# Optimization experiments

Hardware: AMD Instinct MI355X
Metric: run time of the kernel (lower is better)

The kernel has to match this reference:

```python
import jax, jax.numpy as jnp
import numpy as np

N_HEADS = 8
D_K = 64
NEG = 1e9


def setup_inputs() -> dict:
    key = jax.random.key(0)
    k1, k2, k3 = jax.random.split(key, 3)
    B, L, C = 4, 2048, 512
    x = jax.random.normal(k1, (B, L, C), dtype=jnp.float32)
    W_in = jax.random.normal(k2, (C, N_HEADS * D_K * 3), dtype=jnp.float32) * (C ** -0.5)
    b_in = jnp.zeros((N_HEADS * D_K * 3,), dtype=jnp.float32)
    W_out = jax.random.normal(k3, (N_HEADS * D_K, C), dtype=jnp.float32) * ((N_HEADS * D_K) ** -0.5)
    b_out = jnp.zeros((C,), dtype=jnp.float32)
    return {"x": x, "W_in": W_in, "b_in": b_in, "W_out": W_out, "b_out": b_out}


def reference(x, W_in, b_in, W_out, b_out):
    B, L, C = x.shape
    H, Dk = N_HEADS, D_K
    scale = Dk ** -0.5
    qkv = x @ W_in + b_in                       # [B, L, 3*H*Dk]
    qkv = qkv.reshape(B, L, H, 3 * Dk)
    q, k, v = jnp.split(qkv, 3, axis=-1)         # each [B, L, H, Dk]
    attn = jnp.einsum('bihd,bjhd->bijh', q, k) * scale  # [B, L, L, H]
    mask = jnp.tril(jnp.ones((L, L), dtype=x.dtype))[None, :, :, None]
    attn = attn * mask - NEG * (1.0 - mask)
    attn = jax.nn.softmax(attn, axis=2)          # softmax over j
    res = jnp.einsum('bijh,bjhd->bihd', attn, v)  # [B, L, H, Dk]
    res = res.reshape(B, L, H * Dk)
    res = res @ W_out + b_out
    return res + x
```

## Files before the change

kernel.cpp:

```cpp
#include <hip/hip_runtime.h>
#include <hip/hip_bf16.h>
#include <math.h>
#include <cstddef>
#include <cstring>


constexpr int B_SZ  = 4;
constexpr int L_SEQ = 2048;
constexpr int C_DIM = 512;
constexpr int H_N   = 8;
constexpr int DK    = 64;
constexpr int N_QKV = 1536;
constexpr int M_ROWS = B_SZ * L_SEQ;
constexpr float QSCALE = 0.125f * 1.44269504088896f;
constexpr float DEFER_THR = 11.5f;

typedef __attribute__((ext_vector_type(4))) float f32x4;
typedef __attribute__((ext_vector_type(8))) short bf16x8;

static __device__ inline ushort f2bf(float f) {
  unsigned u = __builtin_bit_cast(unsigned, f);
  u += 0x7fffu + ((u >> 16) & 1u);
  return (ushort)(u >> 16);
}

static __device__ inline unsigned pack_bf2(float a, float b) {
  const __hip_bfloat162 v = __float22bfloat162_rn(make_float2(a, b));
  unsigned u;
  __builtin_memcpy(&u, &v, 4);
  return u;
}

typedef __attribute__((address_space(1))) const unsigned int* gas1_t;
typedef __attribute__((address_space(3))) unsigned int* las3_t;
static __device__ inline void gload_lds16(const void* g, void* l) {
  __builtin_amdgcn_global_load_lds((gas1_t)g, (las3_t)l, 16, 0, 0);
}


__global__ __launch_bounds__(256) void convert_bf16(
    const float* __restrict__ src, ushort* __restrict__ dst, int n4) {
  const int i = blockIdx.x * 256 + threadIdx.x;
  if (i < n4) {
    const float4 v = reinterpret_cast<const float4*>(src)[i];
    ushort4 o;
    o.x = f2bf(v.x); o.y = f2bf(v.y); o.z = f2bf(v.z); o.w = f2bf(v.w);
    reinterpret_cast<ushort4*>(dst)[i] = o;
  }
}

__global__ __launch_bounds__(256) void transpose_bf16(
    const float* __restrict__ src, ushort* __restrict__ dst, int R, int C) {
  __shared__ ushort T[64][65];
  const int c0 = blockIdx.x * 64, r0 = blockIdx.y * 64;
#pragma unroll
  for (int p = 0; p < 16; ++p) {
    const int idx = threadIdx.x + p * 256;
    const int r = idx >> 6, c = idx & 63;
    T[r][c] = f2bf(src[(size_t)(r0 + r) * C + c0 + c]);
  }
  __syncthreads();
#pragma unroll
  for (int p = 0; p < 16; ++p) {
    const int idx = threadIdx.x + p * 256;
    const int r = idx >> 6, c = idx & 63;
    dst[(size_t)(c0 + r) * R + r0 + c] = T[c][r];
  }
}

template <int EPI>
__global__ __launch_bounds__(256) void gemm_bf16(
    const ushort* __restrict__ A, const ushort* __restrict__ Bt,
    const float* __restrict__ bias, ushort* __restrict__ Qo,
    ushort* __restrict__ Ko, ushort* __restrict__ Vto,
    float* __restrict__ outF, const float* __restrict__ resid,
    int N, int K) {
  __shared__ ushort Al[128 * 32];
  __shared__ ushort Bl[128 * 32];
  const int tid = threadIdx.x;
  const int w = tid >> 6, l = tid & 63;
  const int cc = l & 15, gg = l >> 4;
  const int bm = blockIdx.y * 128, bn = blockIdx.x * 128;
  const int wr = w >> 1, wc = w & 1;
  f32x4 acc[4][4] = {};

  for (int k0 = 0; k0 < K; k0 += 32) {
#pragma unroll
    for (int q = 0; q < 2; ++q) {
      const int cbase = q * 256 + w * 64;
      const int c = cbase + l;
      gload_lds16(A + (size_t)(bm + (c >> 2)) * K + k0 + (c & 3) * 8,
                  &Al[cbase * 8]);
      gload_lds16(Bt + (size_t)(bn + (c >> 2)) * K + k0 + (c & 3) * 8,
                  &Bl[cbase * 8]);
    }
    __syncthreads();
    bf16x8 aF[4], bF[4];
#pragma unroll
    for (int i = 0; i < 4; ++i)
      aF[i] = *reinterpret_cast<const bf16x8*>(
          &Al[(wr * 64 + i * 16 + cc) * 32 + gg * 8]);
#pragma unroll
    for (int j = 0; j < 4; ++j)
      bF[j] = *reinterpret_cast<const bf16x8*>(
          &Bl[(wc * 64 + j * 16 + cc) * 32 + gg * 8]);
#pragma unroll
    for (int i = 0; i < 4; ++i)
#pragma unroll
      for (int j = 0; j < 4; ++j)
        acc[i][j] = __builtin_amdgcn_mfma_f32_16x16x32_bf16(aF[i], bF[j],
                                                            acc[i][j], 0, 0, 0);
    __syncthreads();
  }

  if (EPI == 0) {
#pragma unroll
    for (int j = 0; j < 4; ++j) {
      const int colbase = bn + wc * 64 + j * 16;
      const int h = colbase / 192, rem = colbase % 192;
      const int type = rem / 64, d = (rem % 64) + cc;
      const float bv = bias[colbase + cc];
#pragma unroll
      for (int i = 0; i < 4; ++i) {
        const int rowbase = bm + wr * 64 + i * 16 + 4 * gg;
        const int b = rowbase >> 11, ll = rowbase & 2047;
        const size_t bh32 = (size_t)(b * H_N + h) * 32;
        if (type == 0) {
#pragma unroll
          for (int r = 0; r < 4; ++r)
            Qo[((size_t)(b * H_N + h) * L_SEQ + ll + r) * DK + d] =
                f2bf((acc[i][j][r] + bv) * QSCALE);
        } else if (type == 1) {
#pragma unroll
          for (int r = 0; r < 4; ++r) {
            const int jg = ll + r;
            Ko[(bh32 + (jg >> 6)) * 4096 + (jg & 63) * 64 +
               (((d >> 3) ^ (jg & 7)) << 3) + (d & 7)] =
                f2bf(acc[i][j][r] + bv);
          }
        } else {
          ushort4 pk;
          pk.x = f2bf(acc[i][j][0] + bv);
          pk.y = f2bf(acc[i][j][1] + bv);
          pk.z = f2bf(acc[i][j][2] + bv);
          pk.w = f2bf(acc[i][j][3] + bv);
          const size_t idx = (bh32 + (ll >> 6)) * 4096 + (size_t)d * 64 +
                             ((((ll & 63) >> 3) ^ (d & 7)) << 3) + (ll & 7);
          *reinterpret_cast<ushort4*>(&Vto[idx]) = pk;
        }
      }
    }
  } else {
#pragma unroll
    for (int j = 0; j < 4; ++j) {
      const int col = bn + wc * 64 + j * 16 + cc;
      const float bv = bias[col];
#pragma unroll
      for (int i = 0; i < 4; ++i) {
        const int rowbase = bm + wr * 64 + i * 16 + 4 * gg;
#pragma unroll
        for (int r = 0; r < 4; ++r) {
          const size_t off = (size_t)(rowbase + r) * N + col;
          outF[off] = acc[i][j][r] + bv + resid[off];
        }
      }
    }
  }
}

#define STAGE(buf, tile)                                                     \
  {                                                                          \
    const ushort* kg_ = KoB + (size_t)(tile) * 4096 + w * 1024 + lane * 8;   \
    const ushort* vg_ = VtB + (size_t)(tile) * 4096 + w * 1024 + lane * 8;   \
    gload_lds16(kg_, &Ks[buf][w * 1024]);                                    \
    gload_lds16(kg_ + 512, &Ks[buf][w * 1024 + 512]);                        \
    gload_lds16(vg_, &Vs[buf][w * 1024]);                                    \
    gload_lds16(vg_ + 512, &Vs[buf][w * 1024 + 512]);                        \
  }

__global__ __launch_bounds__(256, 2) void attn_mfma(
    const ushort* __restrict__ Q, const ushort* __restrict__ Ko,
    const ushort* __restrict__ Vt, ushort* __restrict__ attn_out) {
  __shared__ ushort Ks[2][4096];
  __shared__ ushort Vs[2][4096];
  __shared__ ushort Pw_s[4][1024];
  const int id = blockIdx.x;
  const int bh = (id & 7) + 8 * ((id >> 3) & 3);
  const int pair = (id >> 5) & 15;
  const int tid = threadIdx.x;
  const int w = tid >> 6, lane = tid & 63;
  const int c = lane & 15, g = lane >> 4;
  const int b = bh >> 3, h = bh & 7;
  const ushort* KoB = Ko + (size_t)bh * 32 * 4096;
  const ushort* VtB = Vt + (size_t)bh * 32 * 4096;
  ushort* Pw = Pw_s[w];
  const int pc0 = (g ^ (c & 7)) * 8;
  const int pc1 = ((g + 4) ^ (c & 7)) * 8;
  const f32x4 zero4 = {0.f, 0.f, 0.f, 0.f};

  for (int ps = 0; ps < 2; ++ps) {
    const int qt = ps ? pair : (31 - pair);
    const int q0 = qt * 64 + w * 16;

    bf16x8 qA[2];
    {
      const ushort* qp = Q + ((size_t)bh * L_SEQ + q0 + c) * DK + g * 8;
      qA[0] = *reinterpret_cast<const bf16x8*>(qp);
      qA[1] = *reinterpret_cast<const bf16x8*>(qp + 32);
    }
    f32x4 O[4] = {};
    float mrow[4] = {-INFINITY, -INFINITY, -INFINITY, -INFINITY};
    float lsum[4] = {};

    STAGE(0, 0);
    __syncthreads();

    for (int jt = 0; jt <= qt; ++jt) {
      const int cur = jt & 1;
      if (jt < qt) STAGE(cur ^ 1, jt + 1);
      const ushort* Kc = Ks[cur];
      const ushort* Vc = Vs[cur];
      f32x4 S[4];
#pragma unroll
      for (int n = 0; n < 4; ++n) {
        const bf16x8 k0 = *reinterpret_cast<const bf16x8*>(&Kc[(n * 16 + c) * 64 + pc0]);
        const bf16x8 k1 = *reinterpret_cast<const bf16x8*>(&Kc[(n * 16 + c) * 64 + pc1]);
        S[n] = __builtin_amdgcn_mfma_f32_16x16x32_bf16(qA[0], k0, zero4, 0, 0, 0);
        S[n] = __builtin_amdgcn_mfma_f32_16x16x32_bf16(qA[1], k1, S[n], 0, 0, 0);
      }
      if (jt == qt) {
        const int j0 = jt * 64;
#pragma unroll
        for (int n = 0; n < 4; ++n)
#pragma unroll
          for (int r = 0; r < 4; ++r)
            if ((j0 + n * 16 + c) > (q0 + 4 * g + r)) S[n][r] = -INFINITY;
      }
      float pm[4];
      int exceed = 0;
#pragma unroll
      for (int r = 0; r < 4; ++r) {
        pm[r] = fmaxf(fmaxf(S[0][r], S[1][r]), fmaxf(S[2][r], S[3][r]));
        exceed |= (pm[r] > mrow[r] + DEFER_THR);
      }
      if (__any(exceed)) {
#pragma unroll
        for (int r = 0; r < 4; ++r) {
          float fm = pm[r];
          fm = fmaxf(fm, __shfl_xor(fm, 1, 16));
          fm = fmaxf(fm, __shfl_xor(fm, 2, 16));
          fm = fmaxf(fm, __shfl_xor(fm, 4, 16));
          fm = fmaxf(fm, __shfl_xor(fm, 8, 16));
          const float mnew = fmaxf(mrow[r], fm);
          const float corr = __builtin_exp2f(mrow[r] - mnew);
          lsum[r] *= corr;
#pragma unroll
          for (int t = 0; t < 4; ++t) O[t][r] *= corr;
          mrow[r] = mnew;
        }
      }
#pragma unroll
      for (int n = 0; n < 4; ++n)
#pragma unroll
        for (int r = 0; r < 4; ++r) {
          const float p = __builtin_exp2f(S[n][r] - mrow[r]);
          S[n][r] = p;
          lsum[r] += p;
        }
#pragma unroll
      for (int n = 0; n < 4; ++n)
#pragma unroll
        for (int r = 0; r < 4; r += 2) {
          const unsigned pk = pack_bf2(S[n][r], S[n][r + 1]);
          const int row0 = 4 * g + r, row1 = row0 + 1;
          Pw[row0 * 64 + ((2 * n + (c >> 3)) ^ (row0 & 7)) * 8 + (c & 7)] =
              (ushort)(pk & 0xffffu);
          Pw[row1 * 64 + ((2 * n + (c >> 3)) ^ (row1 & 7)) * 8 + (c & 7)] =
              (ushort)(pk >> 16);
        }
      const bf16x8 pA0 = *reinterpret_cast<const bf16x8*>(&Pw[c * 64 + pc0]);
      const bf16x8 pA1 = *reinterpret_cast<const bf16x8*>(&Pw[c * 64 + pc1]);
#pragma unroll
      for (int t = 0; t < 4; ++t) {
        const bf16x8 v0 = *reinterpret_cast<const bf16x8*>(&Vc[(t * 16 + c) * 64 + pc0]);
        const bf16x8 v1 = *reinterpret_cast<const bf16x8*>(&Vc[(t * 16 + c) * 64 + pc1]);
        O[t] = __builtin_amdgcn_mfma_f32_16x16x32_bf16(pA0, v0, O[t], 0, 0, 0);
        O[t] = __builtin_amdgcn_mfma_f32_16x16x32_bf16(pA1, v1, O[t], 0, 0, 0);
      }
      __syncthreads();
    }
    float inv[4];
#pragma unroll
    for (int r = 0; r < 4; ++r) {
      float s = lsum[r];
      s += __shfl_xor(s, 1, 16);
      s += __shfl_xor(s, 2, 16);
      s += __shfl_xor(s, 4, 16);
      s += __shfl_xor(s, 8, 16);
      inv[r] = 1.f / s;
    }
#pragma unroll
    for (int t = 0; t < 4; ++t)
#pragma unroll
      for (int r = 0; r < 4; ++r)
        attn_out[((size_t)b * L_SEQ + q0 + 4 * g + r) * C_DIM + h * DK + t * 16 + c] =
            f2bf(O[t][r] * inv[r]);
    __syncthreads();
  }
}

extern "C" void kernel_launch(void* const* d_in, const int* in_sizes, int n_in,
                              void* d_out, int out_size, void* d_ws,
                              size_t ws_size, hipStream_t stream) {
  const float* x     = (const float*)d_in[0];
  const float* W_in  = (const float*)d_in[1];
  const float* b_in  = (const float*)d_in[2];
  const float* W_out = (const float*)d_in[3];
  const float* b_out = (const float*)d_in[4];
  float* out = (float*)d_out;

  ushort* xbf   = (ushort*)d_ws;
  ushort* WinT  = xbf + (size_t)M_ROWS * C_DIM;
  ushort* WoutT = WinT + (size_t)N_QKV * C_DIM;
  ushort* Qo    = WoutT + (size_t)C_DIM * C_DIM;
  ushort* Ko    = Qo + (size_t)M_ROWS * C_DIM;
  ushort* Vto   = Ko + (size_t)M_ROWS * C_DIM;
  ushort* attnb = Vto + (size_t)M_ROWS * C_DIM;

  convert_bf16<<<(M_ROWS * C_DIM / 4 + 255) / 256, 256, 0, stream>>>(
      x, xbf, M_ROWS * C_DIM / 4);
  transpose_bf16<<<dim3(N_QKV / 64, C_DIM / 64), 256, 0, stream>>>(
      W_in, WinT, C_DIM, N_QKV);
  transpose_bf16<<<dim3(C_DIM / 64, C_DIM / 64), 256, 0, stream>>>(
      W_out, WoutT, C_DIM, C_DIM);

  gemm_bf16<0><<<dim3(N_QKV / 128, M_ROWS / 128), 256, 0, stream>>>(
      xbf, WinT, b_in, Qo, Ko, Vto, nullptr, nullptr, N_QKV, C_DIM);
  attn_mfma<<<dim3(512, 1, 1), 256, 0, stream>>>(Qo, Ko, Vto, attnb);
  gemm_bf16<1><<<dim3(C_DIM / 128, M_ROWS / 128), 256, 0, stream>>>(
      attnb, WoutT, b_out, nullptr, nullptr, nullptr, out, x, C_DIM, C_DIM);
}
```

Baseline: 104.5 us.

## Rewrite attention with 32x32 MFMA, transposed S, register-resident P

```diff
diff --git a/kernel.cpp b/kernel.cpp
--- a/kernel.cpp
+++ b/kernel.cpp
@@ -16,7 +16,9 @@
 constexpr float DEFER_THR = 11.5f;
 
 typedef __attribute__((ext_vector_type(4))) float f32x4;
+typedef __attribute__((ext_vector_type(16))) float f32x16;
 typedef __attribute__((ext_vector_type(8))) short bf16x8;
+typedef __attribute__((ext_vector_type(4))) unsigned int u32x4;
 
 static __device__ inline ushort f2bf(float f) {
   unsigned u = __builtin_bit_cast(unsigned, f);
@@ -178,135 +180,144 @@
     gload_lds16(vg_ + 512, &Vs[buf][w * 1024 + 512]);                        \
   }
 
-__global__ __launch_bounds__(256, 2) void attn_mfma(
+__global__ __launch_bounds__(256) void attn_mfma32(
     const ushort* __restrict__ Q, const ushort* __restrict__ Ko,
     const ushort* __restrict__ Vt, ushort* __restrict__ attn_out) {
   __shared__ ushort Ks[2][4096];
   __shared__ ushort Vs[2][4096];
-  __shared__ ushort Pw_s[4][1024];
   const int id = blockIdx.x;
   const int bh = (id & 7) + 8 * ((id >> 3) & 3);
-  const int pair = (id >> 5) & 15;
+  const int hi5 = id >> 5;
+  const int qb = (hi5 < 8) ? (15 - hi5) : (hi5 - 8);
   const int tid = threadIdx.x;
   const int w = tid >> 6, lane = tid & 63;
-  const int c = lane & 15, g = lane >> 4;
+  const int ql = lane & 31;
+  const int hi = lane >> 5;
   const int b = bh >> 3, h = bh & 7;
   const ushort* KoB = Ko + (size_t)bh * 32 * 4096;
   const ushort* VtB = Vt + (size_t)bh * 32 * 4096;
-  ushort* Pw = Pw_s[w];
-  const int pc0 = (g ^ (c & 7)) * 8;
-  const int pc1 = ((g + 4) ^ (c & 7)) * 8;
-  const f32x4 zero4 = {0.f, 0.f, 0.f, 0.f};
-
-  for (int ps = 0; ps < 2; ++ps) {
-    const int qt = ps ? pair : (31 - pair);
-    const int q0 = qt * 64 + w * 16;
-
-    bf16x8 qA[2];
-    {
-      const ushort* qp = Q + ((size_t)bh * L_SEQ + q0 + c) * DK + g * 8;
-      qA[0] = *reinterpret_cast<const bf16x8*>(qp);
-      qA[1] = *reinterpret_cast<const bf16x8*>(qp + 32);
-    }
-    f32x4 O[4] = {};
-    float mrow[4] = {-INFINITY, -INFINITY, -INFINITY, -INFINITY};
-    float lsum[4] = {};
-
-    STAGE(0, 0);
-    __syncthreads();
-
-    for (int jt = 0; jt <= qt; ++jt) {
-      const int cur = jt & 1;
-      if (jt < qt) STAGE(cur ^ 1, jt + 1);
+  const int qg = qb * 128 + w * 32 + ql;
+  const int nt = 2 * qb + 2;
+  const int lastw = nt - 2 + (w >> 1);
+
+  bf16x8 qF[4];
+  {
+    const ushort* qp = Q + ((size_t)bh * L_SEQ + qg) * DK + 8 * hi;
+#pragma unroll
+    for (int s = 0; s < 4; ++s)
+      qF[s] = *reinterpret_cast<const bf16x8*>(qp + 16 * s);
+  }
+
+  f32x16 O0 = {}, O1 = {};
+  float mrow = -INFINITY, lsum = 0.f;
+
+  STAGE(0, 0);
+  __syncthreads();
+
+  for (int jt = 0; jt < nt; ++jt) {
+    const int cur = jt & 1;
+    if (jt + 1 < nt) STAGE(cur ^ 1, jt + 1);
+    if (jt <= lastw) {
       const ushort* Kc = Ks[cur];
       const ushort* Vc = Vs[cur];
-      f32x4 S[4];
-#pragma unroll
-      for (int n = 0; n < 4; ++n) {
-        const bf16x8 k0 = *reinterpret_cast<const bf16x8*>(&Kc[(n * 16 + c) * 64 + pc0]);
-        const bf16x8 k1 = *reinterpret_cast<const bf16x8*>(&Kc[(n * 16 + c) * 64 + pc1]);
-        S[n] = __builtin_amdgcn_mfma_f32_16x16x32_bf16(qA[0], k0, zero4, 0, 0, 0);
-        S[n] = __builtin_amdgcn_mfma_f32_16x16x32_bf16(qA[1], k1, S[n], 0, 0, 0);
-      }
-      if (jt == qt) {
+      f32x16 S0 = {}, S1 = {};
+#pragma unroll
+      for (int s = 0; s < 4; ++s) {
+        const int cd = 2 * s + hi;
+        const int ph = (cd ^ (ql & 7)) * 8;
+        const bf16x8 k0 = *reinterpret_cast<const bf16x8*>(&Kc[ql * 64 + ph]);
+        const bf16x8 k1 = *reinterpret_cast<const bf16x8*>(&Kc[(32 + ql) * 64 + ph]);
+        S0 = __builtin_amdgcn_mfma_f32_32x32x16_bf16(k0, qF[s], S0, 0, 0, 0);
+        S1 = __builtin_amdgcn_mfma_f32_32x32x16_bf16(k1, qF[s], S1, 0, 0, 0);
+      }
+      if (jt == lastw) {
         const int j0 = jt * 64;
 #pragma unroll
-        for (int n = 0; n < 4; ++n)
-#pragma unroll
-          for (int r = 0; r < 4; ++r)
-            if ((j0 + n * 16 + c) > (q0 + 4 * g + r)) S[n][r] = -INFINITY;
-      }
-      float pm[4];
-      int exceed = 0;
-#pragma unroll
-      for (int r = 0; r < 4; ++r) {
-        pm[r] = fmaxf(fmaxf(S[0][r], S[1][r]), fmaxf(S[2][r], S[3][r]));
-        exceed |= (pm[r] > mrow[r] + DEFER_THR);
-      }
-      if (__any(exceed)) {
-#pragma unroll
-        for (int r = 0; r < 4; ++r) {
-          float fm = pm[r];
-          fm = fmaxf(fm, __shfl_xor(fm, 1, 16));
-          fm = fmaxf(fm, __shfl_xor(fm, 2, 16));
-          fm = fmaxf(fm, __shfl_xor(fm, 4, 16));
-          fm = fmaxf(fm, __shfl_xor(fm, 8, 16));
-          const float mnew = fmaxf(mrow[r], fm);
-          const float corr = __builtin_exp2f(mrow[r] - mnew);
-          lsum[r] *= corr;
-#pragma unroll
-          for (int t = 0; t < 4; ++t) O[t][r] *= corr;
-          mrow[r] = mnew;
+        for (int r = 0; r < 16; ++r) {
+          const int jm = j0 + (r & 3) + 8 * (r >> 2) + 4 * hi;
+          if (jm > qg) S0[r] = -INFINITY;
+          if (jm + 32 > qg) S1[r] = -INFINITY;
         }
       }
-#pragma unroll
-      for (int n = 0; n < 4; ++n)
-#pragma unroll
-        for (int r = 0; r < 4; ++r) {
-          const float p = __builtin_exp2f(S[n][r] - mrow[r]);
-          S[n][r] = p;
-          lsum[r] += p;
+      float pm = S0[0];
+#pragma unroll
+      for (int r = 1; r < 16; ++r) pm = fmaxf(pm, S0[r]);
+#pragma unroll
+      for (int r = 0; r < 16; ++r) pm = fmaxf(pm, S1[r]);
+      if (__any(pm > mrow + DEFER_THR)) {
+        const float fm = fmaxf(pm, __shfl_xor(pm, 32, 64));
+        const float mnew = fmaxf(mrow, fm);
+        const float corr = __builtin_exp2f(mrow - mnew);
+        lsum *= corr;
+#pragma unroll
+        for (int r = 0; r < 16; ++r) { O0[r] *= corr; O1[r] *= corr; }
+        mrow = mnew;
+      }
+#pragma unroll
+      for (int r = 0; r < 16; ++r) {
+        S0[r] = __builtin_exp2f(S0[r] - mrow); lsum += S0[r];
+        S1[r] = __builtin_exp2f(S1[r] - mrow); lsum += S1[r];
+      }
+      unsigned uA0[4], uA1[4], uB0[4], uB1[4];
+#pragma unroll
+      for (int s = 0; s < 4; ++s) {
+        const int base = 8 * (s & 1);
+        if (s < 2) {
+          uA0[s] = pack_bf2(S0[base + 0], S0[base + 1]);
+          uA1[s] = pack_bf2(S0[base + 2], S0[base + 3]);
+          uB0[s] = pack_bf2(S0[base + 4], S0[base + 5]);
+          uB1[s] = pack_bf2(S0[base + 6], S0[base + 7]);
+        } else {
+          uA0[s] = pack_bf2(S1[base + 0], S1[base + 1]);
+          uA1[s] = pack_bf2(S1[base + 2], S1[base + 3]);
+          uB0[s] = pack_bf2(S1[base + 4], S1[base + 5]);
+          uB1[s] = pack_bf2(S1[base + 6], S1[base + 7]);
         }
-#pragma unroll
-      for (int n = 0; n < 4; ++n)
-#pragma unroll
-        for (int r = 0; r < 4; r += 2) {
-          const unsigned pk = pack_bf2(S[n][r], S[n][r + 1]);
-          const int row0 = 4 * g + r, row1 = row0 + 1;
-          Pw[row0 * 64 + ((2 * n + (c >> 3)) ^ (row0 & 7)) * 8 + (c & 7)] =
-              (ushort)(pk & 0xffffu);
-          Pw[row1 * 64 + ((2 * n + (c >> 3)) ^ (row1 & 7)) * 8 + (c & 7)] =
-              (ushort)(pk >> 16);
-        }
-      const bf16x8 pA0 = *reinterpret_cast<const bf16x8*>(&Pw[c * 64 + pc0]);
-      const bf16x8 pA1 = *reinterpret_cast<const bf16x8*>(&Pw[c * 64 + pc1]);
-#pragma unroll
-      for (int t = 0; t < 4; ++t) {
-        const bf16x8 v0 = *reinterpret_cast<const bf16x8*>(&Vc[(t * 16 + c) * 64 + pc0]);
-        const bf16x8 v1 = *reinterpret_cast<const bf16x8*>(&Vc[(t * 16 + c) * 64 + pc1]);
-        O[t] = __builtin_amdgcn_mfma_f32_16x16x32_bf16(pA0, v0, O[t], 0, 0, 0);
-        O[t] = __builtin_amdgcn_mfma_f32_16x16x32_bf16(pA1, v1, O[t], 0, 0, 0);
-      }
-      __syncthreads();
-    }
-    float inv[4];
-#pragma unroll
-    for (int r = 0; r < 4; ++r) {
-      float s = lsum[r];
-      s += __shfl_xor(s, 1, 16);
-      s += __shfl_xor(s, 2, 16);
-      s += __shfl_xor(s, 4, 16);
-      s += __shfl_xor(s, 8, 16);
-      inv[r] = 1.f / s;
-    }
-#pragma unroll
-    for (int t = 0; t < 4; ++t)
-#pragma unroll
-      for (int r = 0; r < 4; ++r)
-        attn_out[((size_t)b * L_SEQ + q0 + 4 * g + r) * C_DIM + h * DK + t * 16 + c] =
-            f2bf(O[t][r] * inv[r]);
+      }
+#pragma unroll
+      for (int s = 0; s < 4; ++s) {
+        const unsigned t0 = hi ? uA0[s] : uB0[s];
+        const unsigned t1 = hi ? uA1[s] : uB1[s];
+        const unsigned x0 = (unsigned)__shfl_xor((int)t0, 32, 64);
+        const unsigned x1 = (unsigned)__shfl_xor((int)t1, 32, 64);
+        u32x4 pw;
+        pw[0] = hi ? x0 : uA0[s];
+        pw[1] = hi ? x1 : uA1[s];
+        pw[2] = hi ? uB0[s] : x0;
+        pw[3] = hi ? uB1[s] : x1;
+        const bf16x8 pf = __builtin_bit_cast(bf16x8, pw);
+        const int cj = 2 * s + hi;
+        const int ph = (cj ^ (ql & 7)) * 8;
+        const bf16x8 v0 = *reinterpret_cast<const bf16x8*>(&Vc[ql * 64 + ph]);
+        const bf16x8 v1 = *reinterpret_cast<const bf16x8*>(&Vc[(32 + ql) * 64 + ph]);
+        O0 = __builtin_amdgcn_mfma_f32_32x32x16_bf16(v0, pf, O0, 0, 0, 0);
+        O1 = __builtin_amdgcn_mfma_f32_32x32x16_bf16(v1, pf, O1, 0, 0, 0);
+      }
+    }
     __syncthreads();
   }
+
+  const float ls = lsum + __shfl_xor(lsum, 32, 64);
+  const float inv = 1.f / ls;
+  ushort* orow = attn_out + ((size_t)b * L_SEQ + qg) * C_DIM + h * DK;
+#pragma unroll
+  for (int dt = 0; dt < 2; ++dt)
+#pragma unroll
+    for (int m = 0; m < 4; ++m) {
+      ushort4 pk4;
+      if (dt == 0) {
+        pk4.x = f2bf(O0[4 * m + 0] * inv);
+        pk4.y = f2bf(O0[4 * m + 1] * inv);
+        pk4.z = f2bf(O0[4 * m + 2] * inv);
+        pk4.w = f2bf(O0[4 * m + 3] * inv);
+      } else {
+        pk4.x = f2bf(O1[4 * m + 0] * inv);
+        pk4.y = f2bf(O1[4 * m + 1] * inv);
+        pk4.z = f2bf(O1[4 * m + 2] * inv);
+        pk4.w = f2bf(O1[4 * m + 3] * inv);
+      }
+      *reinterpret_cast<ushort4*>(orow + 32 * dt + 8 * m + 4 * hi) = pk4;
+    }
 }
 
 extern "C" void kernel_launch(void* const* d_in, const int* in_sizes, int n_in,
@@ -336,7 +347,7 @@
 
   gemm_bf16<0><<<dim3(N_QKV / 128, M_ROWS / 128), 256, 0, stream>>>(
       xbf, WinT, b_in, Qo, Ko, Vto, nullptr, nullptr, N_QKV, C_DIM);
-  attn_mfma<<<dim3(512, 1, 1), 256, 0, stream>>>(Qo, Ko, Vto, attnb);
+  attn_mfma32<<<dim3(512, 1, 1), 256, 0, stream>>>(Qo, Ko, Vto, attnb);
   gemm_bf16<1><<<dim3(C_DIM / 128, M_ROWS / 128), 256, 0, stream>>>(
       attnb, WoutT, b_out, nullptr, nullptr, nullptr, out, x, C_DIM, C_DIM);
 }
```

Measured after the change: 120.7 us. +15.6%, slower.
